# Kernel tuning notes

Hardware: AMD Instinct MI355X
Metric: run time of the kernel (lower is better)

## Reference

```python
import jax, jax.numpy as jnp
import numpy as np

B, D_MODEL, HID, N_BINS, DEPTH = 524288, 128, 16, 256, 8


def setup_inputs() -> dict:
    key = jax.random.key(0)
    ks = jax.random.split(key, 8)
    s_in = 1.0 / np.sqrt(D_MODEL)
    s_h = 1.0 / np.sqrt(HID)
    return {
        "hidden_state": jax.random.normal(ks[0], (B, D_MODEL), dtype=jnp.float32),
        # params stored as [in, out] so y = x @ W + b (equivalent to torch Linear)
        "W_in": jax.random.uniform(ks[1], (D_MODEL, HID), jnp.float32, -s_in, s_in),
        "b_in": jax.random.uniform(ks[2], (HID,), jnp.float32, -s_in, s_in),
        "embed": jax.random.normal(ks[3], (N_BINS, HID), dtype=jnp.float32),
        "W_mlp": jax.random.uniform(ks[4], (HID, HID), jnp.float32, -s_h, s_h),
        "b_mlp": jax.random.uniform(ks[5], (HID,), jnp.float32, -s_h, s_h),
        "W_out": jax.random.uniform(ks[6], (HID, N_BINS), jnp.float32, -s_h, s_h),
        "b_out": jax.random.uniform(ks[7], (N_BINS,), jnp.float32, -s_h, s_h),
    }


def reference(hidden_state, W_in, b_in, embed, W_mlp, b_mlp, W_out, b_out):
    # eval-mode forward (deterministic argmax path of AddrNet)
    h = hidden_state @ W_in + b_in  # [B, HID]
    bins = []
    for _ in range(DEPTH):  # depth=8: fixed tiny structural loop
        logits = h @ W_out + b_out          # [B, N_BINS]
        idx = jnp.argmax(logits, axis=-1)   # [B] int
        h = h + embed[idx]                  # conditioning on chosen bin
        h = jax.nn.silu(h @ W_mlp + b_mlp)
        bins.append(idx)
    return jnp.stack(bins, axis=1)  # [B, DEPTH] int32/int64 indices
```

## Files before the change

kernel.cpp:

```cpp
#include <hip/hip_runtime.h>
#include <math.h>


constexpr int BATCH  = 524288;
constexpr int DM     = 128;
constexpr int H      = 16;
constexpr int NB     = 256;
constexpr int DEPTHN = 8;

constexpr int BLOCK = 256;
constexpr int STG   = 20;

typedef float v2f    __attribute__((ext_vector_type(2)));
typedef float f32x4  __attribute__((ext_vector_type(4)));
typedef int   i32x4  __attribute__((ext_vector_type(4)));
typedef short bf16x8 __attribute__((ext_vector_type(8)));

__device__ __forceinline__ unsigned bf16_rne(float f) {
    unsigned u = __builtin_bit_cast(unsigned, f);
    return (u + 0x7fffu + ((u >> 16) & 1u)) >> 16;
}
__device__ __forceinline__ float bf16_to_f(unsigned b) {
    return __builtin_bit_cast(float, b << 16);
}

__device__ __forceinline__ float np_expf(float x) {
    const float LOG2E = 1.442695040888963407f;
    const float C1    = 0.693359375f;
    const float C2    = -2.12194440e-4f;
    float q = rintf(x * LOG2E);
    float r = __builtin_fmaf(q, -C1, x);
    r = __builtin_fmaf(q, -C2, r);
    float p = 1.9875691500E-4f;
    p = __builtin_fmaf(p, r, 1.3981999507E-3f);
    p = __builtin_fmaf(p, r, 8.3334519073E-3f);
    p = __builtin_fmaf(p, r, 4.1665795894E-2f);
    p = __builtin_fmaf(p, r, 1.6666665459E-1f);
    p = __builtin_fmaf(p, r, 5.0000001201E-1f);
    p = __builtin_fmaf(p, r * r, r);
    p = p + 1.0f;
    if (x > 88.72283935546875f)      return INFINITY;
    if (x < -103.97208404541015625f) return 0.0f;
    return ldexpf(p, (int)q);
}

__global__ void addrnet_prep_kernel(const float* __restrict__ W_out,
                                    const float* __restrict__ W_mlp,
                                    float* __restrict__ ws) {
    int t = threadIdx.x;
    for (int i = t; i < NB * H; i += 256) {
        int p = i >> 5, r = i & 31;
        int k = r >> 1, hh = r & 1;
        ws[i] = W_out[k * NB + (2 * p + hh)];
    }
    {
        int ii = t >> 4, k = t & 15;
        ws[NB * H + ii * H + k] = W_mlp[k * H + ii];
    }
}

__global__ __launch_bounds__(BLOCK, 2) void addrnet_r18_kernel(
    const float* __restrict__ x,
    const float* __restrict__ W_in,
    const float* __restrict__ b_in,
    const float* __restrict__ embed,
    const float* __restrict__ b_mlp,
    const float* __restrict__ b_out,
    const float* __restrict__ W_out,
    const float* __restrict__ ws,
    int* __restrict__ out)
{
#pragma clang fp contract(off)
    __shared__ __align__(16) int   sA[16][64][4];
    __shared__ __align__(16) int   sStage[4][64 * STG];
    __shared__ __align__(16) float sBias[NB];

    const int tid = threadIdx.x;
    const int ln  = tid & 63;
    const int wid = tid >> 6;

    for (int slot = tid; slot < 16 * 64; slot += BLOCK) {
        int bt = slot >> 6, l = slot & 63;
        int m  = 16 * bt + (l & 15);
        int k0 = (l >> 4) * 8;
        for (int j = 0; j < 4; ++j) {
            unsigned e2[2];
            for (int e = 0; e < 2; ++e) {
                int k  = k0 + 2 * j + e;
                int kk = k & 15;
                float w = W_out[kk * NB + m];
                unsigned whi = bf16_rne(w);
                unsigned wlo = bf16_rne(w - bf16_to_f(whi));
                e2[e] = (k < 16) ? whi : wlo;
            }
            sA[bt][l][j] = (int)(e2[0] | (e2[1] << 16));
        }
    }
    if (tid < NB) sBias[tid] = b_out[tid];
    __syncthreads();

    const float* WM = ws + NB * H;
    const v2f*   WP = reinterpret_cast<const v2f*>(ws);

    const int row = blockIdx.x * BLOCK + tid;

    float h[H];
#pragma unroll
    for (int j = 0; j < H; ++j) h[j] = 0.0f;
    const float4* xr = reinterpret_cast<const float4*>(x + (size_t)row * DM);
    for (int k4 = 0; k4 < DM / 4; ++k4) {
        float4 v = xr[k4];
        const float* w0 = &W_in[(k4 * 4 + 0) * H];
        const float* w1 = &W_in[(k4 * 4 + 1) * H];
        const float* w2 = &W_in[(k4 * 4 + 2) * H];
        const float* w3 = &W_in[(k4 * 4 + 3) * H];
#pragma unroll
        for (int j = 0; j < H; ++j) {
            float a = h[j];
            a = a + v.x * w0[j];
            a = a + v.y * w1[j];
            a = a + v.z * w2[j];
            a = a + v.w * w3[j];
            h[j] = a;
        }
    }
#pragma unroll
    for (int j = 0; j < H; ++j) h[j] = h[j] + b_in[j];

    int* o = out + (size_t)row * DEPTHN;
    int* stme = &sStage[wid][ln * STG];
    const int binbase = (ln >> 4) * 4;

    for (int d = 0; d < DEPTHN; ++d) {
        float m01 = fmaxf(fabsf(h[0]), fabsf(h[1]));
        float m23 = fmaxf(fabsf(h[2]), fabsf(h[3]));
        float m45 = fmaxf(fabsf(h[4]), fabsf(h[5]));
        float m67 = fmaxf(fabsf(h[6]), fabsf(h[7]));
        float m89 = fmaxf(fabsf(h[8]), fabsf(h[9]));
        float mab = fmaxf(fabsf(h[10]), fabsf(h[11]));
        float mcd = fmaxf(fabsf(h[12]), fabsf(h[13]));
        float mef = fmaxf(fabsf(h[14]), fabsf(h[15]));
        float hmax = fmaxf(fmaxf(fmaxf(m01, m23), fmaxf(m45, m67)),
                           fmaxf(fmaxf(m89, mab), fmaxf(mcd, mef)));
        const float EPS2 = 6e-4f * hmax + 1e-5f;

        int dw[16];
#pragma unroll
        for (int i = 0; i < 8; ++i) {
            unsigned a  = bf16_rne(h[2 * i]);
            unsigned b  = bf16_rne(h[2 * i + 1]);
            unsigned la = bf16_rne(h[2 * i]     - bf16_to_f(a));
            unsigned lb = bf16_rne(h[2 * i + 1] - bf16_to_f(b));
            dw[i]     = (int)(a  | (b  << 16));
            dw[8 + i] = (int)(la | (lb << 16));
        }
        {
            i32x4 s0 = {dw[0], dw[1], dw[2], dw[3]};
            i32x4 s1 = {dw[4], dw[5], dw[6], dw[7]};
            i32x4 s2 = {dw[8], dw[9], dw[10], dw[11]};
            i32x4 s3 = {dw[12], dw[13], dw[14], dw[15]};
            *reinterpret_cast<i32x4*>(&stme[0])  = s0;
            *reinterpret_cast<i32x4*>(&stme[4])  = s1;
            *reinterpret_cast<i32x4*>(&stme[8])  = s2;
            *reinterpret_cast<i32x4*>(&stme[12]) = s3;
        }

        bf16x8 bfr[4];
#pragma unroll
        for (int g = 0; g < 4; ++g) {
            const i32x4* p = reinterpret_cast<const i32x4*>(
                &sStage[wid][((ln & 15) + 16 * g) * STG + (ln >> 4) * 4]);
            bfr[g] = __builtin_bit_cast(bf16x8, *p);
        }

        float mx0 = -INFINITY, sec0 = -INFINITY, t30 = -INFINITY; int gb0 = 0, i20 = 0;
        float mx1 = -INFINITY, sec1 = -INFINITY, t31 = -INFINITY; int gb1 = 0, i21 = 0;
        float mx2 = -INFINITY, sec2 = -INFINITY, t32 = -INFINITY; int gb2 = 0, i22 = 0;
        float mx3 = -INFINITY, sec3 = -INFINITY, t33 = -INFINITY; int gb3 = 0, i23 = 0;

#define INS(MX, GB, SEC, I2, T3, V, BIN)                                   \
        {                                                                  \
            float v_ = (V); int b_ = (BIN);                                \
            T3 = fmaxf(T3, fminf(SEC, v_));                                \
            bool c1 = v_ > MX;                                             \
            bool c2 = v_ > SEC;                                            \
            I2 = c1 ? GB : (c2 ? b_ : I2);                                 \
            GB = c1 ? b_ : GB;                                             \
            SEC = __builtin_amdgcn_fmed3f(MX, SEC, v_);                    \
            MX = fmaxf(MX, v_);                                            \
        }

        for (int bt = 0; bt < 16; ++bt) {
            i32x4 a0i = *reinterpret_cast<const i32x4*>(&sA[bt][ln][0]);
            i32x4 a1i = *reinterpret_cast<const i32x4*>(&sA[bt][ln ^ 32][0]);
            bf16x8 a0 = __builtin_bit_cast(bf16x8, a0i);
            bf16x8 a1 = __builtin_bit_cast(bf16x8, a1i);
            f32x4 bias4 = *reinterpret_cast<const f32x4*>(&sBias[16 * bt + binbase]);
            int bin0 = 16 * bt + binbase;
#pragma unroll
            for (int g = 0; g < 4; ++g) {
                f32x4 acc = bias4;
                acc = __builtin_amdgcn_mfma_f32_16x16x32_bf16(a0, bfr[g], acc, 0, 0, 0);
                acc = __builtin_amdgcn_mfma_f32_16x16x32_bf16(a1, bfr[g], acc, 0, 0, 0);
                if (g == 0) {
                    INS(mx0, gb0, sec0, i20, t30, acc[0], bin0 + 0);
                    INS(mx0, gb0, sec0, i20, t30, acc[1], bin0 + 1);
                    INS(mx0, gb0, sec0, i20, t30, acc[2], bin0 + 2);
                    INS(mx0, gb0, sec0, i20, t30, acc[3], bin0 + 3);
                } else if (g == 1) {
                    INS(mx1, gb1, sec1, i21, t31, acc[0], bin0 + 0);
                    INS(mx1, gb1, sec1, i21, t31, acc[1], bin0 + 1);
                    INS(mx1, gb1, sec1, i21, t31, acc[2], bin0 + 2);
                    INS(mx1, gb1, sec1, i21, t31, acc[3], bin0 + 3);
                } else if (g == 2) {
                    INS(mx2, gb2, sec2, i22, t32, acc[0], bin0 + 0);
                    INS(mx2, gb2, sec2, i22, t32, acc[1], bin0 + 1);
                    INS(mx2, gb2, sec2, i22, t32, acc[2], bin0 + 2);
                    INS(mx2, gb2, sec2, i22, t32, acc[3], bin0 + 3);
                } else {
                    INS(mx3, gb3, sec3, i23, t33, acc[0], bin0 + 0);
                    INS(mx3, gb3, sec3, i23, t33, acc[1], bin0 + 1);
                    INS(mx3, gb3, sec3, i23, t33, acc[2], bin0 + 2);
                    INS(mx3, gb3, sec3, i23, t33, acc[3], bin0 + 3);
                }
            }
        }
#undef INS

        float kmx = -INFINITY, ksec = -INFINITY, kt3 = -INFINITY;
        int kgb = 0, ki2 = 0;
#define MERGE_KEEP(MX, GB, SEC, I2, T3, G)                                 \
        {                                                                  \
            float mx_ = MX, sec_ = SEC, t3_ = T3; int gb_ = GB, i2_ = I2;  \
            _Pragma("unroll")                                              \
            for (int s = 16; s <= 32; s <<= 1) {                           \
                float pmx = __shfl_xor(mx_, s);                            \
                int   pgb = __shfl_xor(gb_, s);                            \
                float pse = __shfl_xor(sec_, s);                           \
                int   pi2 = __shfl_xor(i2_, s);                            \
                float pt3 = __shfl_xor(t3_, s);                            \
                bool t  = pmx > mx_;                                       \
                float nmx = t ? pmx : mx_;  int ngb = t ? pgb : gb_;       \
                float lmx = t ? mx_ : pmx;  int lgb = t ? gb_ : pgb;       \
                float wse = t ? pse : sec_; int wsi = t ? pi2 : i2_;       \
                bool u  = lmx > wse;                                       \
                float nse = u ? lmx : wse;  int ni2 = u ? lgb : wsi;       \
                float c3  = u ? wse : lmx;                                 \
                float lse = t ? sec_ : pse;                                \
                float nt3 = fmaxf(fmaxf(c3, lse), fmaxf(t3_, pt3));        \
                mx_ = nmx; gb_ = ngb; sec_ = nse; i2_ = ni2; t3_ = nt3;    \
            }                                                              \
            bool own = ((ln >> 4) == (G));                                 \
            kmx = own ? mx_ : kmx;   kgb = own ? gb_ : kgb;                \
            ksec = own ? sec_ : ksec; ki2 = own ? i2_ : ki2;               \
            kt3 = own ? t3_ : kt3;                                         \
        }
        MERGE_KEEP(mx0, gb0, sec0, i20, t30, 0)
        MERGE_KEEP(mx1, gb1, sec1, i21, t31, 1)
        MERGE_KEEP(mx2, gb2, sec2, i22, t32, 2)
        MERGE_KEEP(mx3, gb3, sec3, i23, t33, 3)
#undef MERGE_KEEP

        int bi;
        if (kmx - kt3 <= EPS2) {
            float bb2 = -INFINITY;
            int bj = 0;
            for (int p = 0; p < NB / 2; ++p) {
                const v2f* wr = &WP[p * H];
                float a0 = 0.0f, a1 = 0.0f;
#pragma unroll
                for (int k = 0; k < H; ++k) {
                    v2f w = wr[k];
                    a0 = a0 + h[k] * w.x;
                    a1 = a1 + h[k] * w.y;
                }
                a0 = a0 + b_out[2 * p];
                a1 = a1 + b_out[2 * p + 1];
                if (a0 > bb2) { bb2 = a0; bj = 2 * p; }
                if (a1 > bb2) { bb2 = a1; bj = 2 * p + 1; }
            }
            bi = bj;
        } else if (kmx - ksec <= EPS2) {
            int lo  = kgb < ki2 ? kgb : ki2;
            int hi2 = kgb < ki2 ? ki2 : kgb;
            float El = 0.0f, Eh = 0.0f;
            {
                const float* wr = ws + (lo >> 1) * 32 + (lo & 1);
#pragma unroll
                for (int k = 0; k < H; ++k) El = El + h[k] * wr[2 * k];
                El = El + b_out[lo];
            }
            {
                const float* wr = ws + (hi2 >> 1) * 32 + (hi2 & 1);
#pragma unroll
                for (int k = 0; k < H; ++k) Eh = Eh + h[k] * wr[2 * k];
                Eh = Eh + b_out[hi2];
            }
            bi = (Eh > El) ? hi2 : lo;
        } else {
            bi = kgb;
        }
        o[d] = bi;

        {
            const float4* e = reinterpret_cast<const float4*>(embed + bi * H);
#pragma unroll
            for (int q4 = 0; q4 < 4; ++q4) {
                float4 ev = e[q4];
                h[q4 * 4 + 0] = h[q4 * 4 + 0] + ev.x;
                h[q4 * 4 + 1] = h[q4 * 4 + 1] + ev.y;
                h[q4 * 4 + 2] = h[q4 * 4 + 2] + ev.z;
                h[q4 * 4 + 3] = h[q4 * 4 + 3] + ev.w;
            }
        }

        float hn[H];
#pragma unroll
        for (int i = 0; i < H; ++i) {
            const float* wr = &WM[i * H];
            float acc = 0.0f;
#pragma unroll
            for (int k = 0; k < H; ++k) acc = acc + h[k] * wr[k];
            acc = acc + b_mlp[i];
            float e = np_expf(-acc);
            float s = 1.0f / (1.0f + e);
            hn[i] = acc * s;
        }
#pragma unroll
        for (int i = 0; i < H; ++i) h[i] = hn[i];
    }
}

extern "C" void kernel_launch(void* const* d_in, const int* in_sizes, int n_in,
                              void* d_out, int out_size, void* d_ws, size_t ws_size,
                              hipStream_t stream) {
    const float* x     = (const float*)d_in[0];
    const float* W_in  = (const float*)d_in[1];
    const float* b_in  = (const float*)d_in[2];
    const float* embed = (const float*)d_in[3];
    const float* W_mlp = (const float*)d_in[4];
    const float* b_mlp = (const float*)d_in[5];
    const float* W_out = (const float*)d_in[6];
    const float* b_out = (const float*)d_in[7];
    int* out  = (int*)d_out;
    float* ws = (float*)d_ws;

    addrnet_prep_kernel<<<1, 256, 0, stream>>>(W_out, W_mlp, ws);

    dim3 grid(BATCH / BLOCK);
    dim3 block(BLOCK);
    addrnet_r18_kernel<<<grid, block, 0, stream>>>(x, W_in, b_in, embed,
                                                   b_mlp, b_out, W_out, ws, out);
}
```

Before: 618.6 us.

## Pack bin index into logit low mantissa bits to simplify top-3 tracking

```diff
diff --git a/kernel.cpp b/kernel.cpp
--- a/kernel.cpp
+++ b/kernel.cpp
@@ -59,7 +59,7 @@
     }
 }
 
-__global__ __launch_bounds__(BLOCK, 2) void addrnet_r18_kernel(
+__global__ __launch_bounds__(BLOCK, 2) void addrnet_r19_kernel(
     const float* __restrict__ x,
     const float* __restrict__ W_in,
     const float* __restrict__ b_in,
@@ -127,9 +127,13 @@
 #pragma unroll
     for (int j = 0; j < H; ++j) h[j] = h[j] + b_in[j];
 
-    int* o = out + (size_t)row * DEPTHN;
     int* stme = &sStage[wid][ln * STG];
+    float* stmef = reinterpret_cast<float*>(stme);
+    const float* swf = reinterpret_cast<const float*>(&sStage[wid][0]);
     const int binbase = (ln >> 4) * 4;
+    const int idq0 = binbase, idq1 = binbase + 1, idq2 = binbase + 2, idq3 = binbase + 3;
+
+    int bins_[DEPTHN];
 
     for (int d = 0; d < DEPTHN; ++d) {
         float m01 = fmaxf(fabsf(h[0]), fabsf(h[1]));
@@ -142,7 +146,11 @@
         float mef = fmaxf(fabsf(h[14]), fabsf(h[15]));
         float hmax = fmaxf(fmaxf(fmaxf(m01, m23), fmaxf(m45, m67)),
                            fmaxf(fmaxf(m89, mab), fmaxf(mcd, mef)));
-        const float EPS2 = 6e-4f * hmax + 1e-5f;
+        float hw = hmax;
+#pragma unroll
+        for (int s = 1; s < 64; s <<= 1) hw = fmaxf(hw, __shfl_xor(hw, s));
+        const float CSH  = 8.0f * hw + 1.0f;
+        const float EPS2 = 4e-3f * hw + 2e-4f;
 
         int dw[16];
 #pragma unroll
@@ -164,6 +172,11 @@
             *reinterpret_cast<i32x4*>(&stme[8])  = s2;
             *reinterpret_cast<i32x4*>(&stme[12]) = s3;
         }
+        {
+            const float4 bb = *reinterpret_cast<const float4*>(&sBias[ln * 4]);
+            float4 bc = {bb.x + CSH, bb.y + CSH, bb.z + CSH, bb.w + CSH};
+            *reinterpret_cast<float4*>(&stmef[16]) = bc;
+        }
 
         bf16x8 bfr[4];
 #pragma unroll
@@ -173,21 +186,19 @@
             bfr[g] = __builtin_bit_cast(bf16x8, *p);
         }
 
-        float mx0 = -INFINITY, sec0 = -INFINITY, t30 = -INFINITY; int gb0 = 0, i20 = 0;
-        float mx1 = -INFINITY, sec1 = -INFINITY, t31 = -INFINITY; int gb1 = 0, i21 = 0;
-        float mx2 = -INFINITY, sec2 = -INFINITY, t32 = -INFINITY; int gb2 = 0, i22 = 0;
-        float mx3 = -INFINITY, sec3 = -INFINITY, t33 = -INFINITY; int gb3 = 0, i23 = 0;
-
-#define INS(MX, GB, SEC, I2, T3, V, BIN)                                   \
+        float p10 = -INFINITY, p20 = -INFINITY, p30 = -INFINITY;
+        float p11 = -INFINITY, p21 = -INFINITY, p31 = -INFINITY;
+        float p12 = -INFINITY, p22 = -INFINITY, p32 = -INFINITY;
+        float p13 = -INFINITY, p23 = -INFINITY, p33 = -INFINITY;
+
+#define SINS(M1, M2, M3, V, IB)                                            \
         {                                                                  \
-            float v_ = (V); int b_ = (BIN);                                \
-            T3 = fmaxf(T3, fminf(SEC, v_));                                \
-            bool c1 = v_ > MX;                                             \
-            bool c2 = v_ > SEC;                                            \
-            I2 = c1 ? GB : (c2 ? b_ : I2);                                 \
-            GB = c1 ? b_ : GB;                                             \
-            SEC = __builtin_amdgcn_fmed3f(MX, SEC, v_);                    \
-            MX = fmaxf(MX, v_);                                            \
+            unsigned sb_ = (__builtin_bit_cast(unsigned, (V)) &            \
+                            0xFFFFFF00u) | (unsigned)(IB);                 \
+            float sv_ = __builtin_bit_cast(float, sb_);                    \
+            M3 = fmaxf(M3, fminf(M2, sv_));                                \
+            M2 = __builtin_amdgcn_fmed3f(M1, M2, sv_);                     \
+            M1 = fmaxf(M1, sv_);                                           \
         }
 
         for (int bt = 0; bt < 16; ++bt) {
@@ -195,71 +206,70 @@
             i32x4 a1i = *reinterpret_cast<const i32x4*>(&sA[bt][ln ^ 32][0]);
             bf16x8 a0 = __builtin_bit_cast(bf16x8, a0i);
             bf16x8 a1 = __builtin_bit_cast(bf16x8, a1i);
-            f32x4 bias4 = *reinterpret_cast<const f32x4*>(&sBias[16 * bt + binbase]);
-            int bin0 = 16 * bt + binbase;
+            f32x4 biasC4 = *reinterpret_cast<const f32x4*>(
+                &swf[(4 * bt + (binbase >> 2)) * STG + 16]);
+            const int ib0 = (bt << 4) | idq0;
+            const int ib1 = (bt << 4) | idq1;
+            const int ib2 = (bt << 4) | idq2;
+            const int ib3 = (bt << 4) | idq3;
 #pragma unroll
             for (int g = 0; g < 4; ++g) {
-                f32x4 acc = bias4;
+                f32x4 acc = biasC4;
                 acc = __builtin_amdgcn_mfma_f32_16x16x32_bf16(a0, bfr[g], acc, 0, 0, 0);
                 acc = __builtin_amdgcn_mfma_f32_16x16x32_bf16(a1, bfr[g], acc, 0, 0, 0);
                 if (g == 0) {
-                    INS(mx0, gb0, sec0, i20, t30, acc[0], bin0 + 0);
-                    INS(mx0, gb0, sec0, i20, t30, acc[1], bin0 + 1);
-                    INS(mx0, gb0, sec0, i20, t30, acc[2], bin0 + 2);
-                    INS(mx0, gb0, sec0, i20, t30, acc[3], bin0 + 3);
+                    SINS(p10, p20, p30, acc[0], ib0);
+                    SINS(p10, p20, p30, acc[1], ib1);
+                    SINS(p10, p20, p30, acc[2], ib2);
+                    SINS(p10, p20, p30, acc[3], ib3);
                 } else if (g == 1) {
-                    INS(mx1, gb1, sec1, i21, t31, acc[0], bin0 + 0);
-                    INS(mx1, gb1, sec1, i21, t31, acc[1], bin0 + 1);
-                    INS(mx1, gb1, sec1, i21, t31, acc[2], bin0 + 2);
-                    INS(mx1, gb1, sec1, i21, t31, acc[3], bin0 + 3);
+                    SINS(p11, p21, p31, acc[0], ib0);
+                    SINS(p11, p21, p31, acc[1], ib1);
+                    SINS(p11, p21, p31, acc[2], ib2);
+                    SINS(p11, p21, p31, acc[3], ib3);
                 } else if (g == 2) {
-                    INS(mx2, gb2, sec2, i22, t32, acc[0], bin0 + 0);
-                    INS(mx2, gb2, sec2, i22, t32, acc[1], bin0 + 1);
-                    INS(mx2, gb2, sec2, i22, t32, acc[2], bin0 + 2);
-                    INS(mx2, gb2, sec2, i22, t32, acc[3], bin0 + 3);
+                    SINS(p12, p22, p32, acc[0], ib0);
+                    SINS(p12, p22, p32, acc[1], ib1);
+                    SINS(p12, p22, p32, acc[2], ib2);
+                    SINS(p12, p22, p32, acc[3], ib3);
                 } else {
-                    INS(mx3, gb3, sec3, i23, t33, acc[0], bin0 + 0);
-                    INS(mx3, gb3, sec3, i23, t33, acc[1], bin0 + 1);
-                    INS(mx3, gb3, sec3, i23, t33, acc[2], bin0 + 2);
-                    INS(mx3, gb3, sec3, i23, t33, acc[3], bin0 + 3);
+                    SINS(p13, p23, p33, acc[0], ib0);
+                    SINS(p13, p23, p33, acc[1], ib1);
+                    SINS(p13, p23, p33, acc[2], ib2);
+                    SINS(p13, p23, p33, acc[3], ib3);
                 }
             }
         }
-#undef INS
+#undef SINS
 
         float kmx = -INFINITY, ksec = -INFINITY, kt3 = -INFINITY;
-        int kgb = 0, ki2 = 0;
-#define MERGE_KEEP(MX, GB, SEC, I2, T3, G)                                 \
+#define MERGE_KEEP(M1, M2, M3, G)                                          \
         {                                                                  \
-            float mx_ = MX, sec_ = SEC, t3_ = T3; int gb_ = GB, i2_ = I2;  \
+            float m1_ = M1, m2_ = M2, m3_ = M3;                            \
             _Pragma("unroll")                                              \
             for (int s = 16; s <= 32; s <<= 1) {                           \
-                float pmx = __shfl_xor(mx_, s);                            \
-                int   pgb = __shfl_xor(gb_, s);                            \
-                float pse = __shfl_xor(sec_, s);                           \
-                int   pi2 = __shfl_xor(i2_, s);                            \
-                float pt3 = __shfl_xor(t3_, s);                            \
-                bool t  = pmx > mx_;                                       \
-                float nmx = t ? pmx : mx_;  int ngb = t ? pgb : gb_;       \
-                float lmx = t ? mx_ : pmx;  int lgb = t ? gb_ : pgb;       \
-                float wse = t ? pse : sec_; int wsi = t ? pi2 : i2_;       \
-                bool u  = lmx > wse;                                       \
-                float nse = u ? lmx : wse;  int ni2 = u ? lgb : wsi;       \
-                float c3  = u ? wse : lmx;                                 \
-                float lse = t ? sec_ : pse;                                \
-                float nt3 = fmaxf(fmaxf(c3, lse), fmaxf(t3_, pt3));        \
-                mx_ = nmx; gb_ = ngb; sec_ = nse; i2_ = ni2; t3_ = nt3;    \
+                float q1 = __shfl_xor(m1_, s);                             \
+                float q2 = __shfl_xor(m2_, s);                             \
+                float q3 = __shfl_xor(m3_, s);                             \
+                float nm1 = fmaxf(m1_, q1);                                \
+                float nm2 = fmaxf(fminf(m1_, q1), fmaxf(m2_, q2));         \
+                float nm3 = fmaxf(fmaxf(fminf(m2_, q1), fminf(m1_, q2)),   \
+                                  fmaxf(m3_, q3));                         \
+                m1_ = nm1; m2_ = nm2; m3_ = nm3;                           \
             }                                                              \
             bool own = ((ln >> 4) == (G));                                 \
-            kmx = own ? mx_ : kmx;   kgb = own ? gb_ : kgb;                \
-            ksec = own ? sec_ : ksec; ki2 = own ? i2_ : ki2;               \
-            kt3 = own ? t3_ : kt3;                                         \
-        }
-        MERGE_KEEP(mx0, gb0, sec0, i20, t30, 0)
-        MERGE_KEEP(mx1, gb1, sec1, i21, t31, 1)
-        MERGE_KEEP(mx2, gb2, sec2, i22, t32, 2)
-        MERGE_KEEP(mx3, gb3, sec3, i23, t33, 3)
+            kmx = own ? m1_ : kmx;                                         \
+            ksec = own ? m2_ : ksec;                                       \
+            kt3 = own ? m3_ : kt3;                                         \
+        }
+        MERGE_KEEP(p10, p20, p30, 0)
+        MERGE_KEEP(p11, p21, p31, 1)
+        MERGE_KEEP(p12, p22, p32, 2)
+        MERGE_KEEP(p13, p23, p33, 3)
 #undef MERGE_KEEP
+
+        int kgb = (int)(__builtin_bit_cast(unsigned, kmx) & 0xFFu);
+        int ki2 = (int)(__builtin_bit_cast(unsigned, ksec) & 0xFFu);
 
         int bi;
         if (kmx - kt3 <= EPS2) {
@@ -300,7 +310,7 @@
         } else {
             bi = kgb;
         }
-        o[d] = bi;
+        bins_[d] = bi;
 
         {
             const float4* e = reinterpret_cast<const float4*>(embed + bi * H);
@@ -329,6 +339,10 @@
 #pragma unroll
         for (int i = 0; i < H; ++i) h[i] = hn[i];
     }
+
+    int* o = out + (size_t)row * DEPTHN;
+    *reinterpret_cast<int4*>(o)     = make_int4(bins_[0], bins_[1], bins_[2], bins_[3]);
+    *reinterpret_cast<int4*>(o + 4) = make_int4(bins_[4], bins_[5], bins_[6], bins_[7]);
 }
 
 extern "C" void kernel_launch(void* const* d_in, const int* in_sizes, int n_in,
@@ -349,6 +363,6 @@
 
     dim3 grid(BATCH / BLOCK);
     dim3 block(BLOCK);
-    addrnet_r18_kernel<<<grid, block, 0, stream>>>(x, W_in, b_in, embed,
+    addrnet_r19_kernel<<<grid, block, 0, stream>>>(x, W_in, b_in, embed,
                                                    b_mlp, b_out, W_out, ws, out);
 }
```

Result: slower. 1.221 ms (+97.4%).
